# Kernel optimization log

Hardware: AMD Instinct MI355X
Metric: run time of the kernel (lower is better)

The kernel has to match this reference:

```python
import jax, jax.numpy as jnp
import numpy as np

V, E, H, B, S = 50000, 512, 1024, 256, 256


def setup_inputs() -> dict:
    key = jax.random.key(0)
    ks = jax.random.split(key, 8)
    inputs = jax.random.randint(ks[0], (B, S), 0, V)
    emb = jax.random.normal(ks[1], (V, E), dtype=jnp.float32)
    sx, sh = 1.0 / np.sqrt(E), 1.0 / np.sqrt(H)  # ~orthogonal column scale
    Wx_f = jax.random.normal(ks[2], (E, 4 * H), dtype=jnp.float32) * sx
    Wh_f = jax.random.normal(ks[3], (H, 4 * H), dtype=jnp.float32) * sh
    Wx_b = jax.random.normal(ks[4], (E, 4 * H), dtype=jnp.float32) * sx
    Wh_b = jax.random.normal(ks[5], (H, 4 * H), dtype=jnp.float32) * sh
    # gate order i, f, o, c ; forget-gate bias initialized to 1 as in the source
    bias = jnp.concatenate([jnp.zeros(H), jnp.ones(H), jnp.zeros(H), jnp.zeros(H)]).astype(jnp.float32)
    W_hq = jax.random.normal(ks[6], (H, 10), dtype=jnp.float32) * sh
    b_q = jnp.zeros(10, dtype=jnp.float32)
    return {"inputs": inputs, "emb": emb, "Wx_f": Wx_f, "Wh_f": Wh_f, "b_f": bias,
            "Wx_b": Wx_b, "Wh_b": Wh_b, "b_b": bias, "W_hq": W_hq, "b_q": b_q}


def _lstm_final_h(x_tbe, Wx, Wh, b):
    """x_tbe: [S,B,E] time-major. Returns final hidden state [B,H]."""
    h0 = jnp.zeros((x_tbe.shape[1], H), dtype=x_tbe.dtype)
    c0 = jnp.zeros_like(h0)

    def cell(carry, X):
        h, c = carry
        g = X @ Wx + h @ Wh + b          # [B, 4H] fused gate pre-activations
        i, f, o, ct = jnp.split(g, 4, axis=-1)
        c = jax.nn.sigmoid(f) * c + jax.nn.sigmoid(i) * jnp.tanh(ct)
        h = jax.nn.sigmoid(o) * jnp.tanh(c)
        return (h, c), None

    (h, _), _ = jax.lax.scan(cell, (h0, c0), x_tbe)
    return h


def reference(inputs, emb, Wx_f, Wh_f, b_f, Wx_b, Wh_b, b_b, W_hq, b_q):
    x = emb[inputs]                      # [B,S,E]
    x = jnp.transpose(x, (1, 0, 2))      # [S,B,E] time-major
    h_fwd = _lstm_final_h(x, Wx_f, Wh_f, b_f)
    h_bwd = _lstm_final_h(x[::-1], Wx_b, Wh_b, b_b)
    logits = (h_fwd + h_bwd) @ W_hq + b_q
    return jax.nn.softmax(logits, axis=1)
```

## Files before the change

### kernel.cpp

```cpp
#include <hip/hip_runtime.h>

#define S_LEN 256
#define BATCH 256
#define EDIM 512
#define HDIM 1024

typedef short short8 __attribute__((ext_vector_type(8)));
typedef float f32x4 __attribute__((ext_vector_type(4)));
typedef unsigned long long u64;

__device__ __forceinline__ unsigned short f2bf(float f) {
  unsigned u = __float_as_uint(f);
  u = u + 0x7FFFu + ((u >> 16) & 1u);
  return (unsigned short)(u >> 16);
}
__device__ __forceinline__ float bf2f(unsigned short s) {
  return __uint_as_float(((unsigned)s) << 16);
}
__device__ __forceinline__ float sigf(float x) { return 1.0f / (1.0f + __expf(-x)); }
__device__ __forceinline__ float tanh_(float x) { return 2.0f / (1.0f + __expf(-2.0f * x)) - 1.0f; }

#define MFMA(d, a, b) d = __builtin_amdgcn_mfma_f32_16x16x32_bf16(a, b, d, 0, 0, 0)

__device__ __forceinline__ short8 load_hfrag(const unsigned short* p) {
  union { u64 d[2]; short8 v; } u;
  u.d[0] = __hip_atomic_load((const u64*)p,       __ATOMIC_RELAXED, __HIP_MEMORY_SCOPE_AGENT);
  u.d[1] = __hip_atomic_load((const u64*)(p + 4), __ATOMIC_RELAXED, __HIP_MEMORY_SCOPE_AGENT);
  return u.v;
}

__global__ void gather_embed(const int* __restrict__ inputs, const float* __restrict__ emb,
                             unsigned short* __restrict__ Xf) {
  int T = blockIdx.x * 256 + threadIdx.x;
  int b  = T & 255;
  int kt = (T >> 8) & 15;
  int s  = T >> 12;
  int vid = inputs[b * S_LEN + s];
  const float* src = emb + (size_t)vid * EDIM + kt * 32;
  unsigned short o[32];
#pragma unroll
  for (int i = 0; i < 32; i += 4) {
    float4 v = *(const float4*)(src + i);
    o[i] = f2bf(v.x); o[i + 1] = f2bf(v.y); o[i + 2] = f2bf(v.z); o[i + 3] = f2bf(v.w);
  }
  uint4* dst = (uint4*)(Xf + (size_t)T * 32);
#pragma unroll
  for (int q = 0; q < 4; ++q) dst[q] = ((const uint4*)o)[q];
}

__global__ void pack_w(const float* __restrict__ Wx_f, const float* __restrict__ Wh_f,
                       const float* __restrict__ Wx_b, const float* __restrict__ Wh_b,
                       unsigned short* __restrict__ Wxp, unsigned short* __restrict__ Whp) {
  __shared__ unsigned short tile[32][68];
  int bid = blockIdx.x;
  int kit = bid % 48;
  int jb  = (bid / 48) & 63;
  int dir = bid / (48 * 64);
  const float* W; int kbase;
  if (kit < 16) { W = dir ? Wx_b : Wx_f; kbase = kit * 32; }
  else          { W = dir ? Wh_b : Wh_f; kbase = (kit - 16) * 32; }
  int t = threadIdx.x;
#pragma unroll
  for (int half = 0; half < 2; ++half) {
    int idx = half * 256 + t;
    int row = idx >> 4;
    int c4  = (idx & 15) << 2;
    int nt  = c4 >> 4;
    int cc  = c4 & 15;
    int n   = nt * 1024 + jb * 16 + cc;
    float4 v = *(const float4*)(W + (size_t)(kbase + row) * 4096 + n);
    tile[row][c4]     = f2bf(v.x); tile[row][c4 + 1] = f2bf(v.y);
    tile[row][c4 + 2] = f2bf(v.z); tile[row][c4 + 3] = f2bf(v.w);
  }
  __syncthreads();
  int nt = t >> 6, cc = (t >> 2) & 15, q = t & 3;
  unsigned short o[8];
#pragma unroll
  for (int e = 0; e < 8; ++e) o[e] = tile[q * 8 + e][nt * 16 + cc];
  size_t unit; unsigned short* dstbase;
  if (kit < 16) { unit = ((size_t)(dir * 64 + jb) * 16 + kit) * 4 + nt;        dstbase = Wxp; }
  else          { unit = ((size_t)(dir * 64 + jb) * 32 + (kit - 16)) * 4 + nt; dstbase = Whp; }
  *(uint4*)(dstbase + unit * 512 + cc * 32 + q * 8) = *(const uint4*)o;
}

__global__ __launch_bounds__(256, 1) void lstm_main(
    const unsigned short* __restrict__ Xf,
    const unsigned short* __restrict__ Wxp,
    const unsigned short* __restrict__ Whp,
    const float* __restrict__ bias_f,
    const float* __restrict__ bias_b,
    unsigned short* __restrict__ Hf,
    unsigned int* __restrict__ slots)
{
  extern __shared__ __align__(16) unsigned char smem[];

  const int bx  = blockIdx.x;
  const int xcd = bx & 7;
  const int dir = xcd >> 2;
  const int mh  = (xcd >> 1) & 1;
  const int jb  = ((xcd & 1) << 5) + (bx >> 3);

  const int tid  = threadIdx.x;
  const int wave = tid >> 6;
  const int lane = tid & 63;
  const int c    = lane & 15;
  const int Q    = lane >> 4;
  const int swc  = (c >> 1) & 3;

  {
    const uint4* src = (const uint4*)Whp + (size_t)(dir * 64 + jb) * 8192;
    for (int i = tid; i < 8192; i += 256) {
      uint4 v = src[i];
      int row = i >> 2, q = i & 3, cc = row & 15;
      *(uint4*)(smem + row * 64 + ((q ^ ((cc >> 1) & 3)) << 4)) = v;
    }
  }
  const float* bias = dir ? bias_b : bias_f;
  const int j = jb * 16 + c;
  float bg[4];
#pragma unroll
  for (int g = 0; g < 4; ++g) bg[g] = bias[g * HDIM + j];
  __syncthreads();

  unsigned int* grp_slots = slots + (dir * 2 + mh) * (64 * 16);
  unsigned int* my_slot   = grp_slots + jb * 16;

  const int arow = (mh * 128 + wave * 32 + c) * 32 + Q * 8;
  const unsigned short* wx_base = Wxp + ((size_t)(dir * 64 + jb) * 16 * 4) * 512 + c * 32 + Q * 8;

  const int kt_j  = j >> 5;
  const int colin = j & 31;

  float c_reg[2][4] = {{0.f,0.f,0.f,0.f},{0.f,0.f,0.f,0.f}};

  for (int s = 0; s < S_LEN; ++s) {
    const int sx = dir ? (S_LEN - 1 - s) : s;
    const int p  = s & 1;

    f32x4 acc[2][4];
#pragma unroll
    for (int mt = 0; mt < 2; ++mt)
#pragma unroll
      for (int g = 0; g < 4; ++g)
        acc[mt][g] = (f32x4){bg[g], bg[g], bg[g], bg[g]};

    {
      const unsigned short* xa = Xf + (size_t)sx * 16 * 8192 + arow;
#pragma unroll 4
      for (int kx = 0; kx < 16; ++kx) {
        short8 a0 = *(const short8*)(xa + kx * 8192);
        short8 a1 = *(const short8*)(xa + kx * 8192 + 512);
        short8 b0 = *(const short8*)(wx_base + (size_t)(kx * 4 + 0) * 512);
        short8 b1 = *(const short8*)(wx_base + (size_t)(kx * 4 + 1) * 512);
        short8 b2 = *(const short8*)(wx_base + (size_t)(kx * 4 + 2) * 512);
        short8 b3 = *(const short8*)(wx_base + (size_t)(kx * 4 + 3) * 512);
        MFMA(acc[0][0], a0, b0); MFMA(acc[0][1], a0, b1);
        MFMA(acc[0][2], a0, b2); MFMA(acc[0][3], a0, b3);
        MFMA(acc[1][0], a1, b0); MFMA(acc[1][1], a1, b1);
        MFMA(acc[1][2], a1, b2); MFMA(acc[1][3], a1, b3);
      }
    }

    if (s > 0) {
      if (tid < 64) {
        const unsigned int* sl = grp_slots + tid * 16;
        for (;;) {
          unsigned v = __hip_atomic_load(sl, __ATOMIC_RELAXED, __HIP_MEMORY_SCOPE_AGENT);
          if (!__any(v < (unsigned)s)) break;
          __builtin_amdgcn_s_sleep(1);
        }
      }
      __syncthreads();
      asm volatile("" ::: "memory");
    }

    {
      const unsigned short* ha = Hf + ((size_t)(p * 2 + dir) * 32) * 8192 + arow;
      short8 pa0[4], pa1[4];
#pragma unroll
      for (int i = 0; i < 4; ++i) {
        pa0[i] = load_hfrag(ha + (size_t)i * 8192);
        pa1[i] = load_hfrag(ha + (size_t)i * 8192 + 512);
      }
#pragma unroll 4
      for (int k = 0; k < 28; ++k) {
        short8 a0 = pa0[k & 3], a1 = pa1[k & 3];
        pa0[k & 3] = load_hfrag(ha + (size_t)(k + 4) * 8192);
        pa1[k & 3] = load_hfrag(ha + (size_t)(k + 4) * 8192 + 512);
        const int rb = (k * 4) * 16 + c;
        short8 b0 = *(const short8*)(smem + (size_t)(rb     ) * 64 + ((Q ^ swc) << 4));
        short8 b1 = *(const short8*)(smem + (size_t)(rb + 16) * 64 + ((Q ^ swc) << 4));
        short8 b2 = *(const short8*)(smem + (size_t)(rb + 32) * 64 + ((Q ^ swc) << 4));
        short8 b3 = *(const short8*)(smem + (size_t)(rb + 48) * 64 + ((Q ^ swc) << 4));
        MFMA(acc[0][0], a0, b0); MFMA(acc[0][1], a0, b1);
        MFMA(acc[0][2], a0, b2); MFMA(acc[0][3], a0, b3);
        MFMA(acc[1][0], a1, b0); MFMA(acc[1][1], a1, b1);
        MFMA(acc[1][2], a1, b2); MFMA(acc[1][3], a1, b3);
      }
#pragma unroll
      for (int k = 28; k < 32; ++k) {
        short8 a0 = pa0[k & 3], a1 = pa1[k & 3];
        const int rb = (k * 4) * 16 + c;
        short8 b0 = *(const short8*)(smem + (size_t)(rb     ) * 64 + ((Q ^ swc) << 4));
        short8 b1 = *(const short8*)(smem + (size_t)(rb + 16) * 64 + ((Q ^ swc) << 4));
        short8 b2 = *(const short8*)(smem + (size_t)(rb + 32) * 64 + ((Q ^ swc) << 4));
        short8 b3 = *(const short8*)(smem + (size_t)(rb + 48) * 64 + ((Q ^ swc) << 4));
        MFMA(acc[0][0], a0, b0); MFMA(acc[0][1], a0, b1);
        MFMA(acc[0][2], a0, b2); MFMA(acc[0][3], a0, b3);
        MFMA(acc[1][0], a1, b0); MFMA(acc[1][1], a1, b1);
        MFMA(acc[1][2], a1, b2); MFMA(acc[1][3], a1, b3);
      }
    }

    {
      unsigned short* hd = Hf + (((size_t)((p ^ 1) * 2 + dir) * 32) + kt_j) * 8192 + colin;
#pragma unroll
      for (int mt = 0; mt < 2; ++mt) {
        const int mrow = mh * 128 + wave * 32 + mt * 16 + Q * 4;
#pragma unroll
        for (int r = 0; r < 4; ++r) {
          float gi = acc[mt][0][r], gf = acc[mt][1][r];
          float go = acc[mt][2][r], gc = acc[mt][3][r];
          float cn = sigf(gf) * c_reg[mt][r] + sigf(gi) * tanh_(gc);
          c_reg[mt][r] = cn;
          __hip_atomic_store(hd + (size_t)(mrow + r) * 32, f2bf(sigf(go) * tanh_(cn)),
                             __ATOMIC_RELAXED, __HIP_MEMORY_SCOPE_AGENT);
        }
      }
    }
    asm volatile("s_waitcnt vmcnt(0)" ::: "memory");
    __syncthreads();
    if (tid == 0)
      __hip_atomic_store(my_slot, (unsigned)(s + 1), __ATOMIC_RELAXED, __HIP_MEMORY_SCOPE_AGENT);
  }
}

__global__ void final_softmax(const unsigned short* __restrict__ Hf,
                              const float* __restrict__ Whq,
                              const float* __restrict__ bq,
                              float* __restrict__ out) {
  __shared__ float red[4][10];
  const int b = blockIdx.x;
  const int tid = threadIdx.x;
  float acc[10];
#pragma unroll
  for (int q = 0; q < 10; ++q) acc[q] = 0.f;
#pragma unroll
  for (int d = 0; d < 2; ++d) {
    const unsigned short* hb = Hf + (size_t)d * 32 * 8192;
#pragma unroll
    for (int u = 0; u < 4; ++u) {
      int jj = tid * 4 + u;
      int kt = jj >> 5, col = jj & 31;
      float xv = bf2f(hb[(size_t)kt * 8192 + b * 32 + col]);
#pragma unroll
      for (int q = 0; q < 10; ++q) acc[q] += xv * Whq[jj * 10 + q];
    }
  }
#pragma unroll
  for (int q = 0; q < 10; ++q)
#pragma unroll
    for (int off = 32; off; off >>= 1) acc[q] += __shfl_down(acc[q], off, 64);
  if ((tid & 63) == 0)
#pragma unroll
    for (int q = 0; q < 10; ++q) red[tid >> 6][q] = acc[q];
  __syncthreads();
  if (tid == 0) {
    float t[10];
#pragma unroll
    for (int q = 0; q < 10; ++q)
      t[q] = red[0][q] + red[1][q] + red[2][q] + red[3][q] + bq[q];
    float mx = t[0];
#pragma unroll
    for (int q = 1; q < 10; ++q) mx = fmaxf(mx, t[q]);
    float sum = 0.f;
#pragma unroll
    for (int q = 0; q < 10; ++q) { t[q] = __expf(t[q] - mx); sum += t[q]; }
    float inv = 1.0f / sum;
#pragma unroll
    for (int q = 0; q < 10; ++q) out[b * 10 + q] = t[q] * inv;
  }
}

extern "C" void kernel_launch(void* const* d_in, const int* in_sizes, int n_in,
                              void* d_out, int out_size, void* d_ws, size_t ws_size,
                              hipStream_t stream) {
  const int*   inputs = (const int*)d_in[0];
  const float* emb    = (const float*)d_in[1];
  const float* Wx_f   = (const float*)d_in[2];
  const float* Wh_f   = (const float*)d_in[3];
  const float* b_f    = (const float*)d_in[4];
  const float* Wx_b   = (const float*)d_in[5];
  const float* Wh_b   = (const float*)d_in[6];
  const float* b_b    = (const float*)d_in[7];
  const float* W_hq   = (const float*)d_in[8];
  const float* b_q    = (const float*)d_in[9];
  float* out = (float*)d_out;

  char* ws = (char*)d_ws;
  unsigned short* Xf  = (unsigned short*)ws;
  unsigned short* Wxp = (unsigned short*)(ws + (64ull << 20));
  unsigned short* Whp = (unsigned short*)(ws + (72ull << 20));
  unsigned short* Hf  = (unsigned short*)(ws + (88ull << 20));
  unsigned int*   slt = (unsigned int*)(ws + (90ull << 20));

  hipMemsetAsync(Hf, 0, (size_t)2 * 2 * 32 * 8192 * sizeof(unsigned short), stream);
  hipMemsetAsync(slt, 0, 4 * 64 * 16 * sizeof(unsigned int), stream);

  gather_embed<<<4096, 256, 0, stream>>>(inputs, emb, Xf);
  pack_w<<<6144, 256, 0, stream>>>(Wx_f, Wh_f, Wx_b, Wh_b, Wxp, Whp);

  hipFuncSetAttribute((const void*)lstm_main,
                      hipFuncAttributeMaxDynamicSharedMemorySize, 131072);

  const unsigned short* xf_p = Xf;
  const unsigned short* wxp_p = Wxp;
  const unsigned short* whp_p = Whp;
  const float* bf_p = b_f;
  const float* bb_p = b_b;
  unsigned short* hf_p = Hf;
  unsigned int* slt_p = slt;
  void* kargs[] = { (void*)&xf_p, (void*)&wxp_p, (void*)&whp_p, (void*)&bf_p,
                    (void*)&bb_p, (void*)&hf_p, (void*)&slt_p };
  hipLaunchCooperativeKernel((void*)lstm_main, dim3(256), dim3(256), kargs, 131072, stream);

  final_softmax<<<256, 256, 0, stream>>>(Hf, W_hq, b_q, out);
}
```

Baseline: 5.132 ms.

## Retile LSTM recurrence to 32-column by 64-row blocks with fragment-native layouts

Each workgroup now owns 32 hidden columns and 64 batch rows (four batch quarters) rather than 16 columns and 128 rows. X, W and H are repacked into MFMA-fragment-native 512-element units so every lane issues one contiguous 16-byte load. Half of the recurrent weight K-range is kept in LDS and the other half is streamed from global/L2 each step, since the doubled column slice no longer fits in LDS. This shrinks sync groups to 32 blocks per direction-quarter and changes the h-exchange layout, at the cost of extra global weight traffic on every time step.

```diff
diff --git a/kernel.cpp b/kernel.cpp
--- a/kernel.cpp
+++ b/kernel.cpp
@@ -4,17 +4,19 @@
 #define BATCH 256
 #define EDIM 512
 #define HDIM 1024
+#define LDS_BYTES 131072
 
 typedef short short8 __attribute__((ext_vector_type(8)));
 typedef float f32x4 __attribute__((ext_vector_type(4)));
 typedef unsigned long long u64;
-
-__device__ __forceinline__ unsigned short f2bf(float f) {
+typedef unsigned short us;
+
+__device__ __forceinline__ us f2bf(float f) {
   unsigned u = __float_as_uint(f);
   u = u + 0x7FFFu + ((u >> 16) & 1u);
-  return (unsigned short)(u >> 16);
-}
-__device__ __forceinline__ float bf2f(unsigned short s) {
+  return (us)(u >> 16);
+}
+__device__ __forceinline__ float bf2f(us s) {
   return __uint_as_float(((unsigned)s) << 16);
 }
 __device__ __forceinline__ float sigf(float x) { return 1.0f / (1.0f + __expf(-x)); }
@@ -22,114 +24,112 @@
 
 #define MFMA(d, a, b) d = __builtin_amdgcn_mfma_f32_16x16x32_bf16(a, b, d, 0, 0, 0)
 
-__device__ __forceinline__ short8 load_hfrag(const unsigned short* p) {
+__device__ __forceinline__ short8 load_hfrag(const us* p) {
   union { u64 d[2]; short8 v; } u;
   u.d[0] = __hip_atomic_load((const u64*)p,       __ATOMIC_RELAXED, __HIP_MEMORY_SCOPE_AGENT);
   u.d[1] = __hip_atomic_load((const u64*)(p + 4), __ATOMIC_RELAXED, __HIP_MEMORY_SCOPE_AGENT);
   return u.v;
 }
+__device__ __forceinline__ short8 ldf(const us* p) {
+  union { uint4 d; short8 v; } u;
+  u.d = *(const uint4*)p;
+  return u.v;
+}
+
 
 __global__ void gather_embed(const int* __restrict__ inputs, const float* __restrict__ emb,
-                             unsigned short* __restrict__ Xf) {
+                             us* __restrict__ Xf) {
   int T = blockIdx.x * 256 + threadIdx.x;
-  int b  = T & 255;
-  int kt = (T >> 8) & 15;
+  int kt = T & 15;
+  int b  = (T >> 4) & 255;
   int s  = T >> 12;
   int vid = inputs[b * S_LEN + s];
   const float* src = emb + (size_t)vid * EDIM + kt * 32;
-  unsigned short o[32];
-#pragma unroll
-  for (int i = 0; i < 32; i += 4) {
-    float4 v = *(const float4*)(src + i);
-    o[i] = f2bf(v.x); o[i + 1] = f2bf(v.y); o[i + 2] = f2bf(v.z); o[i + 3] = f2bf(v.w);
-  }
-  uint4* dst = (uint4*)(Xf + (size_t)T * 32);
-#pragma unroll
-  for (int q = 0; q < 4; ++q) dst[q] = ((const uint4*)o)[q];
+  int c = b & 15;
+  us* ub = Xf + ((size_t)(s * 16 + kt) * 16 + (b >> 4)) * 512;
+#pragma unroll
+  for (int q = 0; q < 4; ++q) {
+    float4 v0 = *(const float4*)(src + q * 8);
+    float4 v1 = *(const float4*)(src + q * 8 + 4);
+    us o[8] = { f2bf(v0.x), f2bf(v0.y), f2bf(v0.z), f2bf(v0.w),
+                f2bf(v1.x), f2bf(v1.y), f2bf(v1.z), f2bf(v1.w) };
+    *(uint4*)(ub + (size_t)(c + 16 * q) * 8) = *(const uint4*)o;
+  }
 }
 
 __global__ void pack_w(const float* __restrict__ Wx_f, const float* __restrict__ Wh_f,
                        const float* __restrict__ Wx_b, const float* __restrict__ Wh_b,
-                       unsigned short* __restrict__ Wxp, unsigned short* __restrict__ Whp) {
-  __shared__ unsigned short tile[32][68];
-  int bid = blockIdx.x;
-  int kit = bid % 48;
-  int jb  = (bid / 48) & 63;
-  int dir = bid / (48 * 64);
-  const float* W; int kbase;
-  if (kit < 16) { W = dir ? Wx_b : Wx_f; kbase = kit * 32; }
-  else          { W = dir ? Wh_b : Wh_f; kbase = (kit - 16) * 32; }
-  int t = threadIdx.x;
-#pragma unroll
-  for (int half = 0; half < 2; ++half) {
-    int idx = half * 256 + t;
-    int row = idx >> 4;
-    int c4  = (idx & 15) << 2;
-    int nt  = c4 >> 4;
-    int cc  = c4 & 15;
-    int n   = nt * 1024 + jb * 16 + cc;
-    float4 v = *(const float4*)(W + (size_t)(kbase + row) * 4096 + n);
-    tile[row][c4]     = f2bf(v.x); tile[row][c4 + 1] = f2bf(v.y);
-    tile[row][c4 + 2] = f2bf(v.z); tile[row][c4 + 3] = f2bf(v.w);
-  }
-  __syncthreads();
-  int nt = t >> 6, cc = (t >> 2) & 15, q = t & 3;
-  unsigned short o[8];
-#pragma unroll
-  for (int e = 0; e < 8; ++e) o[e] = tile[q * 8 + e][nt * 16 + cc];
-  size_t unit; unsigned short* dstbase;
-  if (kit < 16) { unit = ((size_t)(dir * 64 + jb) * 16 + kit) * 4 + nt;        dstbase = Wxp; }
-  else          { unit = ((size_t)(dir * 64 + jb) * 32 + (kit - 16)) * 4 + nt; dstbase = Whp; }
-  *(uint4*)(dstbase + unit * 512 + cc * 32 + q * 8) = *(const uint4*)o;
+                       us* __restrict__ Wxp, us* __restrict__ Whp) {
+  int T = blockIdx.x * 256 + threadIdx.x;
+  int c = T & 15;
+  int q = (T >> 4) & 3;
+  int t = (T >> 6) & 7;
+  int r = T >> 9;
+  int kit = r % 48;
+  int jbd = r / 48;
+  int jb  = jbd & 31;
+  int dir = jbd >> 5;
+  int g = t >> 1, h16 = t & 1;
+  int n = g * 1024 + jb * 32 + h16 * 16 + c;
+  const float* W; int k0;
+  if (kit < 16) { W = dir ? Wx_b : Wx_f; k0 = kit * 32 + q * 8; }
+  else          { W = dir ? Wh_b : Wh_f; k0 = (kit - 16) * 32 + q * 8; }
+  us o[8];
+#pragma unroll
+  for (int e = 0; e < 8; ++e) o[e] = f2bf(W[(size_t)(k0 + e) * 4096 + n]);
+  us* dst;
+  if (kit < 16) dst = Wxp + (((size_t)(dir * 32 + jb) * 16 + kit) * 8 + t) * 512;
+  else          dst = Whp + (((size_t)(dir * 32 + jb) * 32 + (kit - 16)) * 8 + t) * 512;
+  *(uint4*)(dst + (size_t)(c + 16 * q) * 8) = *(const uint4*)o;
 }
 
 __global__ __launch_bounds__(256, 1) void lstm_main(
-    const unsigned short* __restrict__ Xf,
-    const unsigned short* __restrict__ Wxp,
-    const unsigned short* __restrict__ Whp,
+    const us* __restrict__ Xf,
+    const us* __restrict__ Wxp,
+    const us* __restrict__ Whp,
     const float* __restrict__ bias_f,
     const float* __restrict__ bias_b,
-    unsigned short* __restrict__ Hf,
+    us* __restrict__ Hf,
     unsigned int* __restrict__ slots)
 {
   extern __shared__ __align__(16) unsigned char smem[];
 
-  const int bx  = blockIdx.x;
-  const int xcd = bx & 7;
-  const int dir = xcd >> 2;
-  const int mh  = (xcd >> 1) & 1;
-  const int jb  = ((xcd & 1) << 5) + (bx >> 3);
+  const int bx   = blockIdx.x;
+  const int xcd  = bx & 7;
+  const int dir  = xcd >> 2;
+  const int joct = xcd & 3;
+  const int rr   = bx >> 3;
+  const int jb   = joct * 8 + (rr & 7);
+  const int mq   = rr >> 3;
 
   const int tid  = threadIdx.x;
   const int wave = tid >> 6;
   const int lane = tid & 63;
+  const int mw   = wave & 1;
+  const int nw   = wave >> 1;
   const int c    = lane & 15;
-  const int Q    = lane >> 4;
-  const int swc  = (c >> 1) & 3;
+  const int q    = lane >> 4;
+  const int lofs = lane * 8;
 
   {
-    const uint4* src = (const uint4*)Whp + (size_t)(dir * 64 + jb) * 8192;
-    for (int i = tid; i < 8192; i += 256) {
-      uint4 v = src[i];
-      int row = i >> 2, q = i & 3, cc = row & 15;
-      *(uint4*)(smem + row * 64 + ((q ^ ((cc >> 1) & 3)) << 4)) = v;
-    }
+    const uint4* src = (const uint4*)(Whp + (((size_t)(dir * 32 + jb) * 32 + 16) * 8) * 512);
+    for (int i = tid; i < 8192; i += 256) *(uint4*)(smem + (size_t)i * 16) = src[i];
   }
   const float* bias = dir ? bias_b : bias_f;
-  const int j = jb * 16 + c;
+  const int j = jb * 32 + nw * 16 + c;
   float bg[4];
 #pragma unroll
   for (int g = 0; g < 4; ++g) bg[g] = bias[g * HDIM + j];
   __syncthreads();
 
-  unsigned int* grp_slots = slots + (dir * 2 + mh) * (64 * 16);
+  unsigned int* grp_slots = slots + (dir * 4 + mq) * (32 * 16);
   unsigned int* my_slot   = grp_slots + jb * 16;
 
-  const int arow = (mh * 128 + wave * 32 + c) * 32 + Q * 8;
-  const unsigned short* wx_base = Wxp + ((size_t)(dir * 64 + jb) * 16 * 4) * 512 + c * 32 + Q * 8;
-
-  const int kt_j  = j >> 5;
-  const int colin = j & 31;
+  const int bt0 = mq * 4 + mw * 2;
+  const us* xu_base  = Xf + (size_t)bt0 * 512 + lofs;
+  const us* wxu = Wxp + (((size_t)(dir * 32 + jb) * 16) * 8 + nw) * 512 + lofs;
+  const us* whu = Whp + (((size_t)(dir * 32 + jb) * 32) * 8 + nw) * 512 + lofs;
+  const int ldsofs = (nw * 512 + lane * 8) * 2;
 
   float c_reg[2][4] = {{0.f,0.f,0.f,0.f},{0.f,0.f,0.f,0.f}};
 
@@ -145,15 +145,16 @@
         acc[mt][g] = (f32x4){bg[g], bg[g], bg[g], bg[g]};
 
     {
-      const unsigned short* xa = Xf + (size_t)sx * 16 * 8192 + arow;
+      const us* xu = xu_base + (size_t)sx * (16 * 16 * 512);
 #pragma unroll 4
-      for (int kx = 0; kx < 16; ++kx) {
-        short8 a0 = *(const short8*)(xa + kx * 8192);
-        short8 a1 = *(const short8*)(xa + kx * 8192 + 512);
-        short8 b0 = *(const short8*)(wx_base + (size_t)(kx * 4 + 0) * 512);
-        short8 b1 = *(const short8*)(wx_base + (size_t)(kx * 4 + 1) * 512);
-        short8 b2 = *(const short8*)(wx_base + (size_t)(kx * 4 + 2) * 512);
-        short8 b3 = *(const short8*)(wx_base + (size_t)(kx * 4 + 3) * 512);
+      for (int k = 0; k < 16; ++k) {
+        short8 a0 = ldf(xu + (size_t)k * 8192);
+        short8 a1 = ldf(xu + (size_t)k * 8192 + 512);
+        const us* wb = wxu + (size_t)k * 4096;
+        short8 b0 = ldf(wb);
+        short8 b1 = ldf(wb + 1024);
+        short8 b2 = ldf(wb + 2048);
+        short8 b3 = ldf(wb + 3072);
         MFMA(acc[0][0], a0, b0); MFMA(acc[0][1], a0, b1);
         MFMA(acc[0][2], a0, b2); MFMA(acc[0][3], a0, b3);
         MFMA(acc[1][0], a1, b0); MFMA(acc[1][1], a1, b1);
@@ -162,7 +163,7 @@
     }
 
     if (s > 0) {
-      if (tid < 64) {
+      if (tid < 32) {
         const unsigned int* sl = grp_slots + tid * 16;
         for (;;) {
           unsigned v = __hip_atomic_load(sl, __ATOMIC_RELAXED, __HIP_MEMORY_SCOPE_AGENT);
@@ -175,55 +176,72 @@
     }
 
     {
-      const unsigned short* ha = Hf + ((size_t)(p * 2 + dir) * 32) * 8192 + arow;
+      const us* hu = Hf + (((size_t)(p * 2 + dir) * 32) * 16 + bt0) * 512 + lofs;
       short8 pa0[4], pa1[4];
 #pragma unroll
       for (int i = 0; i < 4; ++i) {
-        pa0[i] = load_hfrag(ha + (size_t)i * 8192);
-        pa1[i] = load_hfrag(ha + (size_t)i * 8192 + 512);
+        pa0[i] = load_hfrag(hu + (size_t)i * 8192);
+        pa1[i] = load_hfrag(hu + (size_t)i * 8192 + 512);
       }
 #pragma unroll 4
-      for (int k = 0; k < 28; ++k) {
+      for (int k = 0; k < 16; ++k) {
         short8 a0 = pa0[k & 3], a1 = pa1[k & 3];
-        pa0[k & 3] = load_hfrag(ha + (size_t)(k + 4) * 8192);
-        pa1[k & 3] = load_hfrag(ha + (size_t)(k + 4) * 8192 + 512);
-        const int rb = (k * 4) * 16 + c;
-        short8 b0 = *(const short8*)(smem + (size_t)(rb     ) * 64 + ((Q ^ swc) << 4));
-        short8 b1 = *(const short8*)(smem + (size_t)(rb + 16) * 64 + ((Q ^ swc) << 4));
-        short8 b2 = *(const short8*)(smem + (size_t)(rb + 32) * 64 + ((Q ^ swc) << 4));
-        short8 b3 = *(const short8*)(smem + (size_t)(rb + 48) * 64 + ((Q ^ swc) << 4));
+        pa0[k & 3] = load_hfrag(hu + (size_t)(k + 4) * 8192);
+        pa1[k & 3] = load_hfrag(hu + (size_t)(k + 4) * 8192 + 512);
+        const us* wb = whu + (size_t)k * 4096;
+        short8 b0 = ldf(wb);
+        short8 b1 = ldf(wb + 1024);
+        short8 b2 = ldf(wb + 2048);
+        short8 b3 = ldf(wb + 3072);
         MFMA(acc[0][0], a0, b0); MFMA(acc[0][1], a0, b1);
         MFMA(acc[0][2], a0, b2); MFMA(acc[0][3], a0, b3);
         MFMA(acc[1][0], a1, b0); MFMA(acc[1][1], a1, b1);
         MFMA(acc[1][2], a1, b2); MFMA(acc[1][3], a1, b3);
       }
-#pragma unroll
-      for (int k = 28; k < 32; ++k) {
+#pragma unroll 4
+      for (int k = 16; k < 28; ++k) {
         short8 a0 = pa0[k & 3], a1 = pa1[k & 3];
-        const int rb = (k * 4) * 16 + c;
-        short8 b0 = *(const short8*)(smem + (size_t)(rb     ) * 64 + ((Q ^ swc) << 4));
-        short8 b1 = *(const short8*)(smem + (size_t)(rb + 16) * 64 + ((Q ^ swc) << 4));
-        short8 b2 = *(const short8*)(smem + (size_t)(rb + 32) * 64 + ((Q ^ swc) << 4));
-        short8 b3 = *(const short8*)(smem + (size_t)(rb + 48) * 64 + ((Q ^ swc) << 4));
+        pa0[k & 3] = load_hfrag(hu + (size_t)(k + 4) * 8192);
+        pa1[k & 3] = load_hfrag(hu + (size_t)(k + 4) * 8192 + 512);
+        const unsigned char* lb = smem + (size_t)(k - 16) * 8192 + ldsofs;
+        short8 b0 = *(const short8*)(lb);
+        short8 b1 = *(const short8*)(lb + 2048);
+        short8 b2 = *(const short8*)(lb + 4096);
+        short8 b3 = *(const short8*)(lb + 6144);
         MFMA(acc[0][0], a0, b0); MFMA(acc[0][1], a0, b1);
         MFMA(acc[0][2], a0, b2); MFMA(acc[0][3], a0, b3);
         MFMA(acc[1][0], a1, b0); MFMA(acc[1][1], a1, b1);
         MFMA(acc[1][2], a1, b2); MFMA(acc[1][3], a1, b3);
       }
+#pragma unroll
+      for (int k = 28; k < 32; ++k) {
+        short8 a0 = pa0[k & 3], a1 = pa1[k & 3];
+        const unsigned char* lb = smem + (size_t)(k - 16) * 8192 + ldsofs;
+        short8 b0 = *(const short8*)(lb);
+        short8 b1 = *(const short8*)(lb + 2048);
+        short8 b2 = *(const short8*)(lb + 4096);
+        short8 b3 = *(const short8*)(lb + 6144);
+        MFMA(acc[0][0], a0, b0); MFMA(acc[0][1], a0, b1);
+        MFMA(acc[0][2], a0, b2); MFMA(acc[0][3], a0, b3);
+        MFMA(acc[1][0], a1, b0); MFMA(acc[1][1], a1, b1);
+        MFMA(acc[1][2], a1, b2); MFMA(acc[1][3], a1, b3);
+      }
     }
 
     {
-      unsigned short* hd = Hf + (((size_t)((p ^ 1) * 2 + dir) * 32) + kt_j) * 8192 + colin;
+      const int q2 = nw * 2 + (c >> 3);
+      const int e2 = c & 7;
+      const size_t ob = ((size_t)(((p ^ 1) * 2 + dir) * 32 + jb) * 16 + bt0) * 512;
 #pragma unroll
       for (int mt = 0; mt < 2; ++mt) {
-        const int mrow = mh * 128 + wave * 32 + mt * 16 + Q * 4;
-#pragma unroll
-        for (int r = 0; r < 4; ++r) {
-          float gi = acc[mt][0][r], gf = acc[mt][1][r];
-          float go = acc[mt][2][r], gc = acc[mt][3][r];
-          float cn = sigf(gf) * c_reg[mt][r] + sigf(gi) * tanh_(gc);
-          c_reg[mt][r] = cn;
-          __hip_atomic_store(hd + (size_t)(mrow + r) * 32, f2bf(sigf(go) * tanh_(cn)),
+        us* hd = Hf + ob + (size_t)mt * 512 + (size_t)(16 * q2) * 8 + e2;
+#pragma unroll
+        for (int rg = 0; rg < 4; ++rg) {
+          float gi = acc[mt][0][rg], gf = acc[mt][1][rg];
+          float go = acc[mt][2][rg], gc = acc[mt][3][rg];
+          float cn = sigf(gf) * c_reg[mt][rg] + sigf(gi) * tanh_(gc);
+          c_reg[mt][rg] = cn;
+          __hip_atomic_store(hd + (size_t)(q * 4 + rg) * 8, f2bf(sigf(go) * tanh_(cn)),
                              __ATOMIC_RELAXED, __HIP_MEMORY_SCOPE_AGENT);
         }
       }
@@ -235,7 +253,7 @@
   }
 }
 
-__global__ void final_softmax(const unsigned short* __restrict__ Hf,
+__global__ void final_softmax(const us* __restrict__ Hf,
                               const float* __restrict__ Whq,
                               const float* __restrict__ bq,
                               float* __restrict__ out) {
@@ -244,41 +262,38 @@
   const int tid = threadIdx.x;
   float acc[10];
 #pragma unroll
-  for (int q = 0; q < 10; ++q) acc[q] = 0.f;
-#pragma unroll
-  for (int d = 0; d < 2; ++d) {
-    const unsigned short* hb = Hf + (size_t)d * 32 * 8192;
-#pragma unroll
-    for (int u = 0; u < 4; ++u) {
-      int jj = tid * 4 + u;
-      int kt = jj >> 5, col = jj & 31;
-      float xv = bf2f(hb[(size_t)kt * 8192 + b * 32 + col]);
-#pragma unroll
-      for (int q = 0; q < 10; ++q) acc[q] += xv * Whq[jj * 10 + q];
-    }
-  }
-#pragma unroll
-  for (int q = 0; q < 10; ++q)
-#pragma unroll
-    for (int off = 32; off; off >>= 1) acc[q] += __shfl_down(acc[q], off, 64);
+  for (int qq = 0; qq < 10; ++qq) acc[qq] = 0.f;
+#pragma unroll
+  for (int u = 0; u < 4; ++u) {
+    int j = tid * 4 + u;
+    int kt = j >> 5, q2 = (j & 31) >> 3, e = j & 7;
+    size_t idx = (((size_t)kt * 16 + (b >> 4)) * 512) + ((size_t)((b & 15) + 16 * q2)) * 8 + e;
+    float xv = bf2f(Hf[idx]) + bf2f(Hf[(size_t)32 * 16 * 512 + idx]);
+#pragma unroll
+    for (int qq = 0; qq < 10; ++qq) acc[qq] += xv * Whq[j * 10 + qq];
+  }
+#pragma unroll
+  for (int qq = 0; qq < 10; ++qq)
+#pragma unroll
+    for (int off = 32; off; off >>= 1) acc[qq] += __shfl_down(acc[qq], off, 64);
   if ((tid & 63) == 0)
 #pragma unroll
-    for (int q = 0; q < 10; ++q) red[tid >> 6][q] = acc[q];
+    for (int qq = 0; qq < 10; ++qq) red[tid >> 6][qq] = acc[qq];
   __syncthreads();
   if (tid == 0) {
     float t[10];
 #pragma unroll
-    for (int q = 0; q < 10; ++q)
-      t[q] = red[0][q] + red[1][q] + red[2][q] + red[3][q] + bq[q];
+    for (int qq = 0; qq < 10; ++qq)
+      t[qq] = red[0][qq] + red[1][qq] + red[2][qq] + red[3][qq] + bq[qq];
     float mx = t[0];
 #pragma unroll
-    for (int q = 1; q < 10; ++q) mx = fmaxf(mx, t[q]);
+    for (int qq = 1; qq < 10; ++qq) mx = fmaxf(mx, t[qq]);
     float sum = 0.f;
 #pragma unroll
-    for (int q = 0; q < 10; ++q) { t[q] = __expf(t[q] - mx); sum += t[q]; }
+    for (int qq = 0; qq < 10; ++qq) { t[qq] = __expf(t[qq] - mx); sum += t[qq]; }
     float inv = 1.0f / sum;
 #pragma unroll
-    for (int q = 0; q < 10; ++q) out[b * 10 + q] = t[q] * inv;
+    for (int qq = 0; qq < 10; ++qq) out[b * 10 + qq] = t[qq] * inv;
   }
 }
 
@@ -298,31 +313,31 @@
   float* out = (float*)d_out;
 
   char* ws = (char*)d_ws;
-  unsigned short* Xf  = (unsigned short*)ws;
-  unsigned short* Wxp = (unsigned short*)(ws + (64ull << 20));
-  unsigned short* Whp = (unsigned short*)(ws + (72ull << 20));
-  unsigned short* Hf  = (unsigned short*)(ws + (88ull << 20));
-  unsigned int*   slt = (unsigned int*)(ws + (90ull << 20));
-
-  hipMemsetAsync(Hf, 0, (size_t)2 * 2 * 32 * 8192 * sizeof(unsigned short), stream);
-  hipMemsetAsync(slt, 0, 4 * 64 * 16 * sizeof(unsigned int), stream);
+  us* Xf  = (us*)ws;
+  us* Wxp = (us*)(ws + (64ull << 20));
+  us* Whp = (us*)(ws + (72ull << 20));
+  us* Hf  = (us*)(ws + (88ull << 20));
+  unsigned int* slt = (unsigned int*)(ws + (90ull << 20));
+
+  hipMemsetAsync(Hf, 0, (size_t)2 * 2 * 32 * 16 * 512 * sizeof(us), stream);
+  hipMemsetAsync(slt, 0, 8 * 32 * 16 * sizeof(unsigned int), stream);
 
   gather_embed<<<4096, 256, 0, stream>>>(inputs, emb, Xf);
   pack_w<<<6144, 256, 0, stream>>>(Wx_f, Wh_f, Wx_b, Wh_b, Wxp, Whp);
 
   hipFuncSetAttribute((const void*)lstm_main,
-                      hipFuncAttributeMaxDynamicSharedMemorySize, 131072);
-
-  const unsigned short* xf_p = Xf;
-  const unsigned short* wxp_p = Wxp;
-  const unsigned short* whp_p = Whp;
+                      hipFuncAttributeMaxDynamicSharedMemorySize, LDS_BYTES);
+
+  const us* xf_p = Xf;
+  const us* wxp_p = Wxp;
+  const us* whp_p = Whp;
   const float* bf_p = b_f;
   const float* bb_p = b_b;
-  unsigned short* hf_p = Hf;
+  us* hf_p = Hf;
   unsigned int* slt_p = slt;
   void* kargs[] = { (void*)&xf_p, (void*)&wxp_p, (void*)&whp_p, (void*)&bf_p,
                     (void*)&bb_p, (void*)&hf_p, (void*)&slt_p };
-  hipLaunchCooperativeKernel((void*)lstm_main, dim3(256), dim3(256), kargs, 131072, stream);
+  hipLaunchCooperativeKernel((void*)lstm_main, dim3(256), dim3(256), kargs, LDS_BYTES, stream);
 
   final_softmax<<<256, 256, 0, stream>>>(Hf, W_hq, b_q, out);
 }
```

New measurement: 4.565 ms. 11.1% less time.
